# Optimization experiments

Measured on AMD Instinct MI355X. Metric: run time of the kernel, lower is better.

Reference implementation:

```python
import jax, jax.numpy as jnp
import numpy as np

N, E, D, H, FF = 50000, 1600000, 128, 8, 512
DK = D // H
EPS = 1e-5


def _layernorm(x, g, b):
    mu = jnp.mean(x, axis=-1, keepdims=True)
    var = jnp.mean((x - mu) ** 2, axis=-1, keepdims=True)
    return (x - mu) * jax.lax.rsqrt(var + EPS) * g + b


def setup_inputs() -> dict:
    key = jax.random.key(0)
    ks = jax.random.split(key, 10)
    s = 0.05
    return {
        "h": jax.random.normal(ks[0], (N, D), jnp.float32),
        "src": jax.random.randint(ks[1], (E,), 0, N, jnp.int32),
        "dst": jax.random.randint(ks[2], (E,), 0, N, jnp.int32),
        "Wq": jax.random.normal(ks[3], (D, D), jnp.float32) * s,
        "Wk": jax.random.normal(ks[4], (D, D), jnp.float32) * s,
        "Wv": jax.random.normal(ks[5], (D, D), jnp.float32) * s,
        "Wo": jax.random.normal(ks[6], (D, D), jnp.float32) * s,
        "ln1_g": jnp.ones((D,), jnp.float32),
        "ln1_b": jnp.zeros((D,), jnp.float32),
        "ln2_g": jnp.ones((D,), jnp.float32),
        "ln2_b": jnp.zeros((D,), jnp.float32),
        "W1": jax.random.normal(ks[7], (D, FF), jnp.float32) * s,
        "b1": jnp.zeros((FF,), jnp.float32),
        "W2": jax.random.normal(ks[8], (FF, D), jnp.float32) * s,
        "b2": jnp.zeros((D,), jnp.float32),
    }


def reference(h, src, dst, Wq, Wk, Wv, Wo, ln1_g, ln1_b, ln2_g, ln2_b, W1, b1, W2, b2):
    # QKV projections (bias-free, as in the torch module)
    q = (h @ Wq).reshape(N, H, DK)
    k = (h @ Wk).reshape(N, H, DK)
    v = (h @ Wv).reshape(N, H, DK)

    # masked_mm: per-edge, per-head score  e[m,h] = q[dst[m]] . k[src[m]]
    e = jnp.einsum("ehd,ehd->eh", q[dst], k[src]) / np.sqrt(DK)

    # sparse_softmax: segment softmax over incoming edges of each dst node
    m = jax.ops.segment_max(e, dst, num_segments=N)  # [N, H]
    ex = jnp.exp(e - m[dst])
    denom = jax.ops.segment_sum(ex, dst, num_segments=N)  # [N, H]
    alpha = ex / denom[dst]  # [E, H]

    # vec_spmm: a[n] = sum_{edges m with dst[m]==n} alpha[m] * v[src[m]]
    a = jax.ops.segment_sum(alpha[:, :, None] * v[src], dst, num_segments=N)
    a = a.reshape(N, D)

    o = a @ Wo
    h1 = _layernorm(h + o, ln1_g, ln1_b)
    ffn = jax.nn.relu(h1 @ W1 + b1) @ W2 + b2
    h2 = _layernorm(h1 + ffn, ln2_g, ln2_b)
    return h2
```

## Files before the change

### kernel.cpp

```cpp
#include <hip/hip_runtime.h>
#include <hip/hip_bf16.h>
#include <math.h>

#define D   128
#define FFD 512
#define NPART 8
#define BINB 1024
#define BCAP 768
#define NPROD 32
#define NSUB 32
#define RCAP 320

typedef __attribute__((ext_vector_type(8))) short bf16x8;
typedef __attribute__((ext_vector_type(4))) float f32x4;
typedef __attribute__((ext_vector_type(2))) float f32x2;

static inline size_t align256(size_t x){ return (x + 255) & ~(size_t)255; }

__device__ __forceinline__ float bf2f(unsigned short u){
    union { unsigned int i; float f; } x; x.i = ((unsigned int)u) << 16; return x.f;
}
__device__ __forceinline__ unsigned short f2bf(float f){
    return __builtin_bit_cast(unsigned short, __float2bfloat16(f));
}
__device__ __forceinline__ unsigned char f2fp8(float f){
    return (unsigned char)(__builtin_amdgcn_cvt_pk_fp8_f32(f, f, 0, false) & 0xff);
}

#define DPP_ADD(x, ctrl) do { \
    int yi_ = __builtin_amdgcn_update_dpp(0, __builtin_bit_cast(int, x), ctrl, 0xf, 0xf, true); \
    x += __builtin_bit_cast(float, yi_); } while(0)

__global__ __launch_bounds__(256) void k_bin3(const int* __restrict__ src,
                                              const int* __restrict__ dst, int E, int N,
                                              unsigned long long* __restrict__ pairs,
                                              int* __restrict__ lens,
                                              unsigned long long* __restrict__ spill,
                                              int* __restrict__ qspill){
    __shared__ int lcur[8];
    int tid = threadIdx.x;
    if (tid < 8) lcur[tid] = 0;
    __syncthreads();
    int slice = (N + 7) >> 3;
    int T = gridDim.x * 256;
    unsigned long long* myreg = pairs + (size_t)blockIdx.x * 8 * BCAP;
    for (int i = blockIdx.x*256 + tid; i < E; i += T){
        int d = __builtin_nontemporal_load(&dst[i]);
        int s = __builtin_nontemporal_load(&src[i]);
        int b = min(d / slice, 7);
        unsigned long long pr = ((unsigned long long)(unsigned)d << 32) | (unsigned)s;
        int slot = atomicAdd(&lcur[b], 1);
        if (slot < BCAP) myreg[(size_t)b*BCAP + slot] = pr;
        else { int p = atomicAdd(qspill, 1); spill[p] = pr; }
    }
    __syncthreads();
    if (tid < 8) lens[blockIdx.x*8 + tid] = min(lcur[tid], BCAP);
}

__global__ __launch_bounds__(256) void k_rebin(const unsigned long long* __restrict__ pairs,
                                               const int* __restrict__ lens,
                                               unsigned* __restrict__ pairs2,
                                               int* __restrict__ rlens,
                                               unsigned long long* __restrict__ spill,
                                               int* __restrict__ qspill, int N){
    __shared__ int lcur[NSUB];
    int part = blockIdx.x & 7, ip = blockIdx.x >> 3;
    int tid = threadIdx.x;
    if (tid < NSUB) lcur[tid] = 0;
    __syncthreads();
    int slice = (N + 7) >> 3;
    unsigned subslice = (unsigned)(slice + NSUB - 1) / NSUB;
    int lo_part = part * slice;
    unsigned* outbase = pairs2 + (size_t)(part*NPROD + ip) * NSUB * RCAP;
    for (int seg = ip*(BINB/NPROD); seg < (ip+1)*(BINB/NPROD); ++seg){
        int len = lens[seg*8 + part];
        const unsigned long long* pp = pairs + ((size_t)seg*8 + part)*BCAP;
        for (int i = tid; i < len; i += 256){
            unsigned long long pr = pp[i];
            int d = (int)(pr >> 32);
            unsigned dl = (unsigned)(d - lo_part);
            unsigned sb = dl / subslice;
            int slot = atomicAdd(&lcur[sb], 1);
            if (slot < RCAP)
                outbase[(size_t)sb*RCAP + slot] = ((dl - sb*subslice) << 24) | (unsigned)pr & 0xFFFFFFu
                    ;
            else { int p = atomicAdd(qspill, 1); spill[p] = pr; }
        }
    }
    __syncthreads();
    if (tid < NSUB) rlens[(part*NPROD + ip)*NSUB + tid] = min(lcur[tid], RCAP);
}

__global__ __launch_bounds__(256) void k_count4(const unsigned* __restrict__ pairs2,
                                                const int* __restrict__ rlens,
                                                const unsigned long long* __restrict__ spill,
                                                const int* __restrict__ qspill,
                                                int* __restrict__ cnt, int N){
    __shared__ int hist[256];
    int part = blockIdx.x & 7, s = blockIdx.x >> 3;
    int slice = (N + 7) >> 3;
    int subslice = (slice + NSUB - 1) / NSUB;
    int lo_part = part*slice;
    int lo = lo_part + s*subslice;
    int part_end = min(lo_part + slice, N);
    int n_sub = max(0, min(subslice, part_end - lo));
    for (int i = threadIdx.x; i < 256; i += 256) hist[i] = 0;
    __syncthreads();
    for (int ip = 0; ip < NPROD; ++ip){
        int r = (part*NPROD + ip)*NSUB + s;
        int len = rlens[r];
        const unsigned* pp = pairs2 + (size_t)r*RCAP;
        for (int i = threadIdx.x; i < len; i += 256)
            atomicAdd(&hist[pp[i] >> 24], 1);
    }
    int ns = *qspill;
    for (int i = threadIdx.x; i < ns; i += 256){
        int r = (int)(spill[i] >> 32) - lo;
        if (r >= 0 && r < n_sub) atomicAdd(&hist[r], 1);
    }
    __syncthreads();
    for (int i = threadIdx.x; i < n_sub; i += 256) cnt[lo + i] = hist[i];
}

__global__ __launch_bounds__(256) void k_scatter4(const unsigned* __restrict__ pairs2,
                                                  const int* __restrict__ rlens,
                                                  const unsigned long long* __restrict__ spill,
                                                  const int* __restrict__ qspill,
                                                  const int* __restrict__ off,
                                                  int* __restrict__ csr_src, int N){
    __shared__ int curl[256];
    int part = blockIdx.x & 7, s = blockIdx.x >> 3;
    int slice = (N + 7) >> 3;
    int subslice = (slice + NSUB - 1) / NSUB;
    int lo_part = part*slice;
    int lo = lo_part + s*subslice;
    int part_end = min(lo_part + slice, N);
    int n_sub = max(0, min(subslice, part_end - lo));
    for (int i = threadIdx.x; i < n_sub; i += 256) curl[i] = off[lo + i];
    __syncthreads();
    for (int ip = 0; ip < NPROD; ++ip){
        int r = (part*NPROD + ip)*NSUB + s;
        int len = rlens[r];
        const unsigned* pp = pairs2 + (size_t)r*RCAP;
        for (int i = threadIdx.x; i < len; i += 256){
            unsigned e = pp[i];
            int pos = atomicAdd(&curl[e >> 24], 1);
            csr_src[pos] = (int)(e & 0xFFFFFFu);
        }
    }
    int ns = *qspill;
    for (int i = threadIdx.x; i < ns; i += 256){
        unsigned long long pr = spill[i];
        int r = (int)(pr >> 32) - lo;
        if (r >= 0 && r < n_sub){
            int pos = atomicAdd(&curl[r], 1);
            csr_src[pos] = (int)(unsigned)pr;
        }
    }
}

__global__ __launch_bounds__(256) void k_bsum(const int* __restrict__ cnt, int N,
                                              int* __restrict__ bsum){
    int id = blockIdx.x*256 + threadIdx.x;
    int v = (id < N) ? cnt[id] : 0;
    #pragma unroll
    for (int o = 1; o < 64; o <<= 1) v += __shfl_xor(v, o);
    __shared__ int w4[4];
    if ((threadIdx.x & 63) == 0) w4[threadIdx.x >> 6] = v;
    __syncthreads();
    if (threadIdx.x == 0) bsum[blockIdx.x] = w4[0] + w4[1] + w4[2] + w4[3];
}

__global__ __launch_bounds__(1024) void k_scanb(const int* __restrict__ bsum, int NB,
                                                int* __restrict__ ebase,
                                                int* __restrict__ off, int N){
    __shared__ int sh[1024];
    int tid = threadIdx.x;
    int v = (tid < NB) ? bsum[tid] : 0;
    sh[tid] = v; __syncthreads();
    for (int o = 1; o < 1024; o <<= 1){
        int t = (tid >= o) ? sh[tid-o] : 0;
        __syncthreads();
        sh[tid] += t;
        __syncthreads();
    }
    if (tid < NB) ebase[tid] = sh[tid] - v;
    if (tid == NB-1) off[N] = sh[tid];
}

__global__ __launch_bounds__(256) void k_off(const int* __restrict__ cnt, int N,
                                             const int* __restrict__ ebase,
                                             int* __restrict__ off){
    __shared__ int sh[256];
    int tid = threadIdx.x;
    int id = blockIdx.x*256 + tid;
    int v = (id < N) ? cnt[id] : 0;
    sh[tid] = v; __syncthreads();
    for (int o = 1; o < 256; o <<= 1){
        int t = (tid >= o) ? sh[tid-o] : 0;
        __syncthreads();
        sh[tid] += t;
        __syncthreads();
    }
    int excl = sh[tid] - v;
    int base = ebase[blockIdx.x];
    if (id < N) off[id] = base + excl;
}

__global__ __launch_bounds__(256) void k_cast(const float* __restrict__ x,
                                              __hip_bfloat16* __restrict__ y, int n4){
    int i = blockIdx.x*blockDim.x + threadIdx.x;
    if (i >= n4) return;
    float4 f = ((const float4*)x)[i];
    ushort4 u;
    u.x = f2bf(f.x); u.y = f2bf(f.y);
    u.z = f2bf(f.z); u.w = f2bf(f.w);
    ((ushort4*)y)[i] = u;
}

__global__ __launch_bounds__(256) void k_prep_all(
    const float* __restrict__ Wq, const float* __restrict__ Wk,
    const float* __restrict__ Wv, const float* __restrict__ Wo,
    const float* __restrict__ W1, const float* __restrict__ W2,
    __hip_bfloat16* __restrict__ Wqkvt, __hip_bfloat16* __restrict__ Wot,
    __hip_bfloat16* __restrict__ W1t,   __hip_bfloat16* __restrict__ W2t){
    const float* W; __hip_bfloat16* Wt; int K, Nc;
    int y = blockIdx.y;
    switch (y){
        case 0: W = Wq; Wt = Wqkvt; K = 128; Nc = 128; break;
        case 1: W = Wk; Wt = Wqkvt; K = 128; Nc = 128; break;
        case 2: W = Wv; Wt = Wqkvt; K = 128; Nc = 128; break;
        case 3: W = Wo; Wt = Wot;   K = 128; Nc = 128; break;
        case 4: W = W1; Wt = W1t;   K = 128; Nc = 512; break;
        default: W = W2; Wt = W2t;  K = 512; Nc = 128; break;
    }
    int total = K*Nc;
    for (int id = blockIdx.x*256 + threadIdx.x; id < total; id += 256*gridDim.x){
        int n = id / K, kk = id % K;
        size_t drow;
        if (y == 1)      drow = 128 + ((n>>1)<<2) + (n&1);
        else if (y == 2) drow = 128 + ((n>>1)<<2) + 2 + (n&1);
        else             drow = n;
        Wt[drow*K + kk] = __float2bfloat16(W[(size_t)kk*Nc + n]);
    }
}

#define BM 128
#define BN 128
#define BK 64

__device__ __forceinline__ bool tile_coords(int M, int &r0, int &c0){
    int ncols = gridDim.x;
    int f = blockIdx.y * ncols + blockIdx.x;
    int xcd = f & 7, s = f >> 3;
    int c = s % ncols, rl = s / ncols;
    int r = rl*8 + xcd;
    r0 = r*BM; c0 = c*BN;
    return r0 < M;
}

__device__ __forceinline__ void stage_tile(const __hip_bfloat16* __restrict__ src,
                                           int row_base, int row_limit, int K, int k0,
                                           __hip_bfloat16* lds){
    int tid = threadIdx.x;
    int wave = tid >> 6;
    #pragma unroll
    for (int i = 0; i < 4; ++i){
        int c = i*256 + tid;
        int r = c >> 3, s = c & 7;
        int sg = s ^ (r & 7);
        int gr = row_base + r; if (gr >= row_limit) gr = row_limit - 1;
        const __hip_bfloat16* gp = src + (size_t)gr*K + k0 + sg*8;
        char* lp = (char*)lds + (i*256 + wave*64)*16;
        __builtin_amdgcn_global_load_lds((const __attribute__((address_space(1))) void*)gp,
                                         (__attribute__((address_space(3))) void*)lp,
                                         16, 0, 0);
    }
}

template<int MODE>
__global__ __launch_bounds__(256) void k_gemm(
    const __hip_bfloat16* __restrict__ A,
    const __hip_bfloat16* __restrict__ Bt,
    int M, int Nc, int K,
    const float* __restrict__ bias, int relu,
    __hip_bfloat16* __restrict__ Cb,
    __hip_bfloat16* __restrict__ qb, unsigned char* __restrict__ kvq,
    const float* __restrict__ resid_f, const __hip_bfloat16* __restrict__ resid_b,
    const float* __restrict__ lg, const float* __restrict__ lb,
    float* __restrict__ yf, __hip_bfloat16* __restrict__ yb){
    __shared__ __hip_bfloat16 As[BM*BK];
    __shared__ __hip_bfloat16 Bs[BN*BK];
    __shared__ float red[2][BM][2];
    int r0, c0;
    if (!tile_coords(M, r0, c0)) return;
    int tid = threadIdx.x;
    int lane = tid & 63, wave = tid >> 6;
    int wr = wave >> 1, wc = wave & 1;
    int lr = lane & 15, ls = lane >> 4;

    f32x4 acc[4][4];
    #pragma unroll
    for (int m = 0; m < 4; m++)
        #pragma unroll
        for (int n = 0; n < 4; n++) acc[m][n] = (f32x4){0.f,0.f,0.f,0.f};

    for (int k0 = 0; k0 < K; k0 += BK){
        stage_tile(A,  r0, M,  K, k0, As);
        stage_tile(Bt, c0, Nc, K, k0, Bs);
        __syncthreads();
        #pragma unroll
        for (int kk = 0; kk < 2; ++kk){
            bf16x8 af[4], bfg[4];
            #pragma unroll
            for (int m = 0; m < 4; m++){
                int R = wr*64 + m*16 + lr;
                int sl = (kk*4 + ls) ^ (R & 7);
                af[m] = *(const bf16x8*)((const char*)As + R*128 + sl*16);
            }
            #pragma unroll
            for (int n = 0; n < 4; n++){
                int R = wc*64 + n*16 + lr;
                int sl = (kk*4 + ls) ^ (R & 7);
                bfg[n] = *(const bf16x8*)((const char*)Bs + R*128 + sl*16);
            }
            #pragma unroll
            for (int m = 0; m < 4; m++)
                #pragma unroll
                for (int n = 0; n < 4; n++)
                    acc[m][n] = __builtin_amdgcn_mfma_f32_16x16x32_bf16(af[m], bfg[n], acc[m][n], 0, 0, 0);
        }
        __syncthreads();
    }

    if (MODE == 0){
        #pragma unroll
        for (int n = 0; n < 4; n++){
            int col = c0 + wc*64 + n*16 + lr;
            float bval = bias ? bias[col] : 0.f;
            #pragma unroll
            for (int m = 0; m < 4; m++){
                #pragma unroll
                for (int j = 0; j < 4; j++){
                    int row = r0 + wr*64 + m*16 + ls*4 + j;
                    if (row >= M) continue;
                    float v = acc[m][n][j] + bval;
                    if (relu) v = fmaxf(v, 0.f);
                    Cb[(size_t)row*Nc + col] = __float2bfloat16(v);
                }
            }
        }
    } else if (MODE == 1){
        int region = c0 >> 7;
        #pragma unroll
        for (int n = 0; n < 4; n++){
            int c16 = wc*64 + n*16 + lr;
            #pragma unroll
            for (int m = 0; m < 4; m++){
                #pragma unroll
                for (int j = 0; j < 4; j++){
                    int row = r0 + wr*64 + m*16 + ls*4 + j;
                    if (row >= M) continue;
                    float v = acc[m][n][j];
                    if (region == 0)
                        ((unsigned short*)qb)[(size_t)row*128 + c16] = f2bf(v);
                    else
                        kvq[(size_t)row*256 + (region-1)*128 + c16] = f2fp8(v);
                }
            }
        }
    } else {
        #pragma unroll
        for (int m = 0; m < 4; m++){
            #pragma unroll
            for (int j = 0; j < 4; j++){
                int row = r0 + wr*64 + m*16 + ls*4 + j;
                float s = 0.f, q = 0.f;
                if (row < M){
                    #pragma unroll
                    for (int n = 0; n < 4; n++){
                        int col = wc*64 + n*16 + lr;
                        float bval = bias ? bias[col] : 0.f;
                        float rv = (MODE == 2) ? resid_f[(size_t)row*128 + col]
                                               : bf2f(((const unsigned short*)resid_b)[(size_t)row*128 + col]);
                        float v = acc[m][n][j] + bval + rv;
                        acc[m][n][j] = v;
                        s += v; q += v*v;
                    }
                }
                #pragma unroll
                for (int o = 1; o < 16; o <<= 1){
                    s += __shfl_xor(s, o);
                    q += __shfl_xor(q, o);
                }
                if (lr == 0 && row < M){
                    int rloc = wr*64 + m*16 + ls*4 + j;
                    red[0][rloc][wc] = s;
                    red[1][rloc][wc] = q;
                }
            }
        }
        __syncthreads();
        #pragma unroll
        for (int m = 0; m < 4; m++){
            #pragma unroll
            for (int j = 0; j < 4; j++){
                int rloc = wr*64 + m*16 + ls*4 + j;
                int row = r0 + rloc;
                if (row >= M) continue;
                float mu  = (red[0][rloc][0] + red[0][rloc][1]) * (1.f/128.f);
                float eq  = (red[1][rloc][0] + red[1][rloc][1]) * (1.f/128.f);
                float var = fmaxf(eq - mu*mu, 0.f);
                float inv = rsqrtf(var + 1e-5f);
                #pragma unroll
                for (int n = 0; n < 4; n++){
                    int col = wc*64 + n*16 + lr;
                    float o = (acc[m][n][j] - mu)*inv*lg[col] + lb[col];
                    if (MODE == 3) yf[(size_t)row*128 + col] = o;
                    else           yb[(size_t)row*128 + col] = __float2bfloat16(o);
                }
            }
        }
    }
}

#define EDGE(u_, dd, axx, ayy) { \
    int s_ = __builtin_amdgcn_readlane(myidx, j+(u_)); \
    unsigned uu = kv[(size_t)(unsigned)s_*64 + lane]; \
    f32x2 kf = __builtin_amdgcn_cvt_pk_f32_fp8((int)uu, false); \
    f32x2 vf = __builtin_amdgcn_cvt_pk_f32_fp8((int)uu, true); \
    float p_ = qx*kf[0] + qy*kf[1]; \
    DPP_ADD(p_, 0xB1); DPP_ADD(p_, 0x4E); DPP_ADD(p_, 0x141); \
    float w_ = __builtin_amdgcn_exp2f(p_); \
    dd += w_; axx = fmaf(w_, vf[0], axx); ayy = fmaf(w_, vf[1], ayy); }

__global__ __launch_bounds__(256) void k_attn(const __hip_bfloat16* __restrict__ qb,
                                              const unsigned* __restrict__ kvq,
                                              const int* __restrict__ off,
                                              const int* __restrict__ csr_src,
                                              __hip_bfloat16* __restrict__ a, int N){
    int wid = (blockIdx.x*blockDim.x + threadIdx.x) >> 6;
    int lane = threadIdx.x & 63;
    if (wid >= N) return;
    ushort2 qu = ((const ushort2*)qb)[(size_t)wid*64 + lane];
    const float SC = 0.25f * 1.44269504f;
    float qx = bf2f(qu.x)*SC, qy = bf2f(qu.y)*SC;
    const unsigned* kv = kvq;
    int beg = off[wid], end = off[wid+1];
    float d0 = 0.f, d1 = 0.f, ax0 = 0.f, ay0 = 0.f, ax1 = 0.f, ay1 = 0.f;
    for (int e0 = beg; e0 < end; e0 += 64){
        int myidx = (e0 + lane < end) ? csr_src[e0 + lane] : 0;
        int cnt = min(64, end - e0);
        int j = 0;
        for (; j + 7 < cnt; j += 8){
            EDGE(0, d0, ax0, ay0); EDGE(1, d1, ax1, ay1);
            EDGE(2, d0, ax0, ay0); EDGE(3, d1, ax1, ay1);
            EDGE(4, d0, ax0, ay0); EDGE(5, d1, ax1, ay1);
            EDGE(6, d0, ax0, ay0); EDGE(7, d1, ax1, ay1);
        }
        for (; j < cnt; ++j){
            EDGE(0, d0, ax0, ay0);
        }
    }
    float dsum = d0 + d1;
    float r = (dsum > 0.f) ? 1.f/dsum : 0.f;
    __hip_bfloat162 o2;
    o2.x = __float2bfloat16((ax0 + ax1)*r);
    o2.y = __float2bfloat16((ay0 + ay1)*r);
    ((__hip_bfloat162*)(a + (size_t)wid*D))[lane] = o2;
}

extern "C" void kernel_launch(void* const* d_in, const int* in_sizes, int n_in,
                              void* d_out, int out_size, void* d_ws, size_t ws_size,
                              hipStream_t stream){
    const float* h    = (const float*)d_in[0];
    const int*   src  = (const int*)  d_in[1];
    const int*   dst  = (const int*)  d_in[2];
    const float* Wq   = (const float*)d_in[3];
    const float* Wk   = (const float*)d_in[4];
    const float* Wv   = (const float*)d_in[5];
    const float* Wo   = (const float*)d_in[6];
    const float* ln1g = (const float*)d_in[7];
    const float* ln1b = (const float*)d_in[8];
    const float* ln2g = (const float*)d_in[9];
    const float* ln2b = (const float*)d_in[10];
    const float* W1   = (const float*)d_in[11];
    const float* b1   = (const float*)d_in[12];
    const float* W2   = (const float*)d_in[13];
    const float* b2   = (const float*)d_in[14];
    float* out = (float*)d_out;

    const int N = in_sizes[0] / D;
    const int E = in_sizes[1];

    char* ws = (char*)d_ws;
    size_t o = 0;
    const size_t row_bf = align256((size_t)N * D * sizeof(__hip_bfloat16));
    const size_t kv_q   = align256((size_t)N * 256);
    const size_t t1_bf  = align256((size_t)N * FFD * sizeof(__hip_bfloat16));

    __hip_bfloat16* qb  = (__hip_bfloat16*)(ws + o); o += row_bf;
    unsigned char* kvq  = (unsigned char*)(ws + o); o += kv_q;
    __hip_bfloat16* ab  = (__hip_bfloat16*)(ws + o); o += row_bf;
    __hip_bfloat16* hb  = (__hip_bfloat16*)(ws + o); o += row_bf;
    __hip_bfloat16* h1b = hb;
    __hip_bfloat16* t1b = (__hip_bfloat16*)(ws + o); o += t1_bf;
    __hip_bfloat16* Wqkvt = (__hip_bfloat16*)(ws + o); o += align256(384*128*2);
    __hip_bfloat16* W1t   = (__hip_bfloat16*)(ws + o); o += align256(512*128*2);
    __hip_bfloat16* W2t   = (__hip_bfloat16*)(ws + o); o += align256(128*512*2);
    __hip_bfloat16* Wot   = (__hip_bfloat16*)(ws + o); o += align256(128*128*2);
    int* cnt   = (int*)(ws + o); o += align256((size_t)N*4);
    int* offp  = (int*)(ws + o); o += align256((size_t)(N+1)*4);
    int* bsum  = (int*)(ws + o); o += align256(1024*4);
    int* ebase = (int*)(ws + o); o += align256(1024*4);
    int* lens  = (int*)(ws + o); o += align256((size_t)BINB*8*4);
    int* rlens = (int*)(ws + o); o += align256((size_t)NPART*NPROD*NSUB*4);
    int* qspill= (int*)(ws + o); o += align256(256);
    int* csr   = (int*)(ws + o); o += align256((size_t)E*4);
    unsigned long long* pairs = (unsigned long long*)(ws + o);
    o += align256((size_t)BINB * 8 * BCAP * 8);
    unsigned* pairs2 = (unsigned*)(ws + o);
    o += align256((size_t)NPART * NPROD * NSUB * RCAP * 4);
    unsigned long long* spill = (unsigned long long*)(ws + o);
    o += align256((size_t)E * 8);

    const int NB = (N + 255)/256;

    (void)hipMemsetAsync(qspill, 0, 256, stream);
    k_bin3<<<BINB, 256, 0, stream>>>(src, dst, E, N, pairs, lens, spill, qspill);

    k_cast<<<(N*D/4 + 255)/256, 256, 0, stream>>>(h, hb, N*D/4);
    k_prep_all<<<dim3(64, 6), 256, 0, stream>>>(Wq, Wk, Wv, Wo, W1, W2,
                                                Wqkvt, Wot, W1t, W2t);

    k_rebin<<<NPART*NPROD, 256, 0, stream>>>(pairs, lens, pairs2, rlens, spill, qspill, N);
    k_count4<<<NPART*NSUB, 256, 0, stream>>>(pairs2, rlens, spill, qspill, cnt, N);
    k_bsum <<<NB, 256, 0, stream>>>(cnt, N, bsum);
    k_scanb<<<1, 1024, 0, stream>>>(bsum, NB, ebase, offp, N);
    k_off  <<<NB, 256, 0, stream>>>(cnt, N, ebase, offp);
    k_scatter4<<<NPART*NSUB, 256, 0, stream>>>(pairs2, rlens, spill, qspill, offp, csr, N);

    int mb = (N + BM - 1)/BM;
    int mb_pad = ((mb + 7)/8)*8;

    k_gemm<1><<<dim3(3, mb_pad), 256, 0, stream>>>(hb, Wqkvt, N, 384, 128,
        nullptr, 0, nullptr, qb, kvq, nullptr, nullptr, nullptr, nullptr, nullptr, nullptr);

    k_attn<<<(N*64 + 255)/256, 256, 0, stream>>>(qb, (const unsigned*)kvq, offp, csr, ab, N);

    k_gemm<2><<<dim3(1, mb_pad), 256, 0, stream>>>(ab, Wot, N, 128, 128,
        nullptr, 0, nullptr, nullptr, nullptr, h, nullptr, ln1g, ln1b, nullptr, h1b);

    k_gemm<0><<<dim3(4, mb_pad), 256, 0, stream>>>(h1b, W1t, N, 512, 128,
        b1, 1, t1b, nullptr, nullptr, nullptr, nullptr, nullptr, nullptr, nullptr, nullptr);

    k_gemm<3><<<dim3(1, mb_pad), 256, 0, stream>>>(t1b, W2t, N, 128, 512,
        b2, 0, nullptr, nullptr, nullptr, nullptr, h1b, ln2g, ln2b, out, nullptr);
}
```

Measured before the change: 243.6 us.

## Process two edges per wavefront in attention with 4-dim lanes and 8-byte KV loads

New measurement: 242.3 us. About the same (-0.5%).

```diff
diff --git a/kernel.cpp b/kernel.cpp
--- a/kernel.cpp
+++ b/kernel.cpp
@@ -82,8 +82,7 @@
             unsigned sb = dl / subslice;
             int slot = atomicAdd(&lcur[sb], 1);
             if (slot < RCAP)
-                outbase[(size_t)sb*RCAP + slot] = ((dl - sb*subslice) << 24) | (unsigned)pr & 0xFFFFFFu
-                    ;
+                outbase[(size_t)sb*RCAP + slot] = ((dl - sb*subslice) << 24) | (unsigned)pr & 0xFFFFFFu;
             else { int p = atomicAdd(qspill, 1); spill[p] = pr; }
         }
     }
@@ -238,8 +237,8 @@
     for (int id = blockIdx.x*256 + threadIdx.x; id < total; id += 256*gridDim.x){
         int n = id / K, kk = id % K;
         size_t drow;
-        if (y == 1)      drow = 128 + ((n>>1)<<2) + (n&1);
-        else if (y == 2) drow = 128 + ((n>>1)<<2) + 2 + (n&1);
+        if (y == 1)      drow = 128 + 8*(n>>2) + (n&3);
+        else if (y == 2) drow = 128 + 8*(n>>2) + 4 + (n&3);
         else             drow = n;
         Wt[drow*K + kk] = __float2bfloat16(W[(size_t)kk*Nc + n]);
     }
@@ -424,50 +423,79 @@
     }
 }
 
-#define EDGE(u_, dd, axx, ayy) { \
-    int s_ = __builtin_amdgcn_readlane(myidx, j+(u_)); \
-    unsigned uu = kv[(size_t)(unsigned)s_*64 + lane]; \
-    f32x2 kf = __builtin_amdgcn_cvt_pk_f32_fp8((int)uu, false); \
-    f32x2 vf = __builtin_amdgcn_cvt_pk_f32_fp8((int)uu, true); \
-    float p_ = qx*kf[0] + qy*kf[1]; \
-    DPP_ADD(p_, 0xB1); DPP_ADD(p_, 0x4E); DPP_ADD(p_, 0x141); \
+#define PAIR(jj, dd, b0, b1, b2, b3) { \
+    int s0_ = __builtin_amdgcn_readlane(myidx, (jj)); \
+    int s1_ = __builtin_amdgcn_readlane(myidx, (jj)+1); \
+    int sv_ = half ? s1_ : s0_; \
+    uint2 u_ = kv[(size_t)(unsigned)sv_*32 + l32]; \
+    f32x2 k01 = __builtin_amdgcn_cvt_pk_f32_fp8((int)u_.x, false); \
+    f32x2 k23 = __builtin_amdgcn_cvt_pk_f32_fp8((int)u_.x, true); \
+    f32x2 v01 = __builtin_amdgcn_cvt_pk_f32_fp8((int)u_.y, false); \
+    f32x2 v23 = __builtin_amdgcn_cvt_pk_f32_fp8((int)u_.y, true); \
+    float p_ = q0*k01[0] + q1*k01[1] + q2*k23[0] + q3*k23[1]; \
+    DPP_ADD(p_, 0xB1); DPP_ADD(p_, 0x4E); \
     float w_ = __builtin_amdgcn_exp2f(p_); \
-    dd += w_; axx = fmaf(w_, vf[0], axx); ayy = fmaf(w_, vf[1], ayy); }
+    dd += w_; \
+    b0 = fmaf(w_, v01[0], b0); b1 = fmaf(w_, v01[1], b1); \
+    b2 = fmaf(w_, v23[0], b2); b3 = fmaf(w_, v23[1], b3); }
+
+#define PAIRV(jj, dd, b0, b1, b2, b3) { \
+    int s0_ = __builtin_amdgcn_readlane(myidx, (jj)); \
+    int s1_ = __builtin_amdgcn_readlane(myidx, min((jj)+1, 63)); \
+    int sv_ = half ? s1_ : s0_; \
+    uint2 u_ = kv[(size_t)(unsigned)sv_*32 + l32]; \
+    f32x2 k01 = __builtin_amdgcn_cvt_pk_f32_fp8((int)u_.x, false); \
+    f32x2 k23 = __builtin_amdgcn_cvt_pk_f32_fp8((int)u_.x, true); \
+    f32x2 v01 = __builtin_amdgcn_cvt_pk_f32_fp8((int)u_.y, false); \
+    f32x2 v23 = __builtin_amdgcn_cvt_pk_f32_fp8((int)u_.y, true); \
+    float p_ = q0*k01[0] + q1*k01[1] + q2*k23[0] + q3*k23[1]; \
+    DPP_ADD(p_, 0xB1); DPP_ADD(p_, 0x4E); \
+    float w_ = __builtin_amdgcn_exp2f(p_); \
+    if ((jj) + half >= cnt) w_ = 0.f; \
+    dd += w_; \
+    b0 = fmaf(w_, v01[0], b0); b1 = fmaf(w_, v01[1], b1); \
+    b2 = fmaf(w_, v23[0], b2); b3 = fmaf(w_, v23[1], b3); }
 
 __global__ __launch_bounds__(256) void k_attn(const __hip_bfloat16* __restrict__ qb,
-                                              const unsigned* __restrict__ kvq,
+                                              const uint2* __restrict__ kv,
                                               const int* __restrict__ off,
                                               const int* __restrict__ csr_src,
                                               __hip_bfloat16* __restrict__ a, int N){
     int wid = (blockIdx.x*blockDim.x + threadIdx.x) >> 6;
     int lane = threadIdx.x & 63;
     if (wid >= N) return;
-    ushort2 qu = ((const ushort2*)qb)[(size_t)wid*64 + lane];
+    int half = lane >> 5, l32 = lane & 31;
+    ushort4 qu = ((const ushort4*)(qb + (size_t)wid*128))[l32];
     const float SC = 0.25f * 1.44269504f;
-    float qx = bf2f(qu.x)*SC, qy = bf2f(qu.y)*SC;
-    const unsigned* kv = kvq;
+    float q0 = bf2f(qu.x)*SC, q1 = bf2f(qu.y)*SC, q2 = bf2f(qu.z)*SC, q3 = bf2f(qu.w)*SC;
     int beg = off[wid], end = off[wid+1];
-    float d0 = 0.f, d1 = 0.f, ax0 = 0.f, ay0 = 0.f, ax1 = 0.f, ay1 = 0.f;
+    float dA=0, a0A=0, a1A=0, a2A=0, a3A=0;
+    float dB=0, a0B=0, a1B=0, a2B=0, a3B=0;
     for (int e0 = beg; e0 < end; e0 += 64){
         int myidx = (e0 + lane < end) ? csr_src[e0 + lane] : 0;
         int cnt = min(64, end - e0);
         int j = 0;
-        for (; j + 7 < cnt; j += 8){
-            EDGE(0, d0, ax0, ay0); EDGE(1, d1, ax1, ay1);
-            EDGE(2, d0, ax0, ay0); EDGE(3, d1, ax1, ay1);
-            EDGE(4, d0, ax0, ay0); EDGE(5, d1, ax1, ay1);
-            EDGE(6, d0, ax0, ay0); EDGE(7, d1, ax1, ay1);
-        }
-        for (; j < cnt; ++j){
-            EDGE(0, d0, ax0, ay0);
-        }
-    }
-    float dsum = d0 + d1;
-    float r = (dsum > 0.f) ? 1.f/dsum : 0.f;
-    __hip_bfloat162 o2;
-    o2.x = __float2bfloat16((ax0 + ax1)*r);
-    o2.y = __float2bfloat16((ay0 + ay1)*r);
-    ((__hip_bfloat162*)(a + (size_t)wid*D))[lane] = o2;
+        for (; j + 3 < cnt; j += 4){
+            PAIR(j,   dA, a0A, a1A, a2A, a3A);
+            PAIR(j+2, dB, a0B, a1B, a2B, a3B);
+        }
+        for (; j < cnt; j += 2){
+            PAIRV(j, dA, a0A, a1A, a2A, a3A);
+        }
+    }
+    float d  = dA + dB;
+    float a0 = a0A + a0B, a1 = a1A + a1B, a2 = a2A + a2B, a3 = a3A + a3B;
+    d  += __shfl_xor(d, 32);
+    a0 += __shfl_xor(a0, 32);
+    a1 += __shfl_xor(a1, 32);
+    a2 += __shfl_xor(a2, 32);
+    a3 += __shfl_xor(a3, 32);
+    if (half == 0){
+        float r = (d > 0.f) ? 1.f/d : 0.f;
+        ushort4 o;
+        o.x = f2bf(a0*r); o.y = f2bf(a1*r); o.z = f2bf(a2*r); o.w = f2bf(a3*r);
+        ((ushort4*)(a + (size_t)wid*128))[l32] = o;
+    }
 }
 
 extern "C" void kernel_launch(void* const* d_in, const int* in_sizes, int n_in,
@@ -546,7 +574,7 @@
     k_gemm<1><<<dim3(3, mb_pad), 256, 0, stream>>>(hb, Wqkvt, N, 384, 128,
         nullptr, 0, nullptr, qb, kvq, nullptr, nullptr, nullptr, nullptr, nullptr, nullptr);
 
-    k_attn<<<(N*64 + 255)/256, 256, 0, stream>>>(qb, (const unsigned*)kvq, offp, csr, ab, N);
+    k_attn<<<(N*64 + 255)/256, 256, 0, stream>>>(qb, (const uint2*)kvq, offp, csr, ab, N);
 
     k_gemm<2><<<dim3(1, mb_pad), 256, 0, stream>>>(ab, Wot, N, 128, 128,
         nullptr, 0, nullptr, nullptr, nullptr, h, nullptr, ln1g, ln1b, nullptr, h1b);
```
